# Kernel tuning notes

Hardware: AMD Instinct MI355X
Metric: run time of the kernel (lower is better)

Reference implementation:

```python
import jax, jax.numpy as jnp
import numpy as np

# Block-diagonal SplitMLP: fc1 group g sees [day | items[g]]; fc2 is purely per-group.
B, C, V, H, O, G = 128, 16, 32, 64, 4, 10000


def setup_inputs() -> dict:
    key = jax.random.key(0)
    ks = jax.random.split(key, 7)
    bound1 = 1.0 / np.sqrt(C + V * G)   # nn.Linear init bound for fc1 (full fan-in)
    bound2 = 1.0 / np.sqrt(H * G)       # fc2 fan-in
    return {
        "day": jax.random.normal(ks[0], (B, C), jnp.float32),
        "items": jax.random.normal(ks[1], (B, G, V), jnp.float32),
        "W1_day": jax.random.uniform(ks[2], (G, H, C), jnp.float32, -bound1, bound1),
        "W1_var": jax.random.uniform(ks[3], (G, H, V), jnp.float32, -bound1, bound1),
        "b1": jax.random.uniform(ks[4], (G, H), jnp.float32, -bound1, bound1),
        "W2": jax.random.uniform(ks[5], (G, O, H), jnp.float32, -bound2, bound2),
        "b2": jax.random.uniform(ks[6], (G, O), jnp.float32, -bound2, bound2),
    }


def reference(day, items, W1_day, W1_var, b1, W2, b2):
    # fc1: shared day columns + per-group var block, then ReLU
    h = (
        jnp.einsum("bc,ghc->bgh", day, W1_day)
        + jnp.einsum("bgv,ghv->bgh", items, W1_var)
        + b1
    )
    h = jax.nn.relu(h)
    # fc2: purely block-diagonal (num_const = 0)
    y = jnp.einsum("bgh,goh->bgo", h, W2) + b2  # (B, G, O)
    return y
```

## Files before the change

kernel.cpp:

```cpp
#include <hip/hip_runtime.h>
#include <hip/hip_bf16.h>


typedef __bf16 v8bf __attribute__((ext_vector_type(8)));
typedef __bf16 v4bf __attribute__((ext_vector_type(4)));
typedef float  v4f  __attribute__((ext_vector_type(4)));

#define B_   128
#define C_   16
#define V_   32
#define H_   64
#define O_   4
#define G_   10000
#define GPB  4
#define WS_  56
#define HS_  72
#define YS_  20

__device__ __forceinline__ v4bf cvt4(float4 f) {
  v4bf r;
  r[0] = (__bf16)f.x; r[1] = (__bf16)f.y; r[2] = (__bf16)f.z; r[3] = (__bf16)f.w;
  return r;
}
__device__ __forceinline__ v8bf cvt8(float4 lo, float4 hi) {
  v8bf r;
  r[0] = (__bf16)lo.x; r[1] = (__bf16)lo.y; r[2] = (__bf16)lo.z; r[3] = (__bf16)lo.w;
  r[4] = (__bf16)hi.x; r[5] = (__bf16)hi.y; r[6] = (__bf16)hi.z; r[7] = (__bf16)hi.w;
  return r;
}
__device__ __forceinline__ v8bf gload8(const float* __restrict__ p) {
  const float4* p4 = reinterpret_cast<const float4*>(p);
  return cvt8(p4[0], p4[1]);
}

__global__ __launch_bounds__(256, 4)
void splitmlp_kernel(const float* __restrict__ day,
                     const float* __restrict__ items,
                     const float* __restrict__ W1d,
                     const float* __restrict__ W1v,
                     const float* __restrict__ b1,
                     const float* __restrict__ W2,
                     const float* __restrict__ b2,
                     float* __restrict__ out) {
  __shared__ __bf16 W1s[H_ * WS_];
  __shared__ __bf16 Hb[4][32 * HS_];
  __shared__ float  Yb[B_ * YS_];

  const int t    = threadIdx.x;
  const int g0   = blockIdx.x * GPB;
  const int w    = t >> 6;
  const int lane = t & 63;
  const int c    = lane & 15;
  const int q    = lane >> 4;
  const int wbase = w * 32;

  v8bf zf;
#pragma unroll
  for (int i = 0; i < 8; ++i) zf[i] = (__bf16)0.0f;
  const v4f zero = {0.f, 0.f, 0.f, 0.f};

  float4 pd, pv0, pv1;
  {
    const float* W1dg = W1d + (size_t)g0 * (H_ * C_);
    const float* W1vg = W1v + (size_t)g0 * (H_ * V_);
    pd  = reinterpret_cast<const float4*>(W1dg)[t];
    pv0 = reinterpret_cast<const float4*>(W1vg)[t];
    pv1 = reinterpret_cast<const float4*>(W1vg)[t + 256];
  }

#pragma unroll 1
  for (int gi = 0; gi < GPB; ++gi) {
    const int g = g0 + gi;

    __syncthreads();
    {
      const int hd = t >> 2, kd = (t & 3) << 2;
      *reinterpret_cast<v4bf*>(&W1s[hd * WS_ + kd]) = cvt4(pd);
      const int hv0 = t >> 3, kv0 = C_ + ((t & 7) << 2);
      *reinterpret_cast<v4bf*>(&W1s[hv0 * WS_ + kv0]) = cvt4(pv0);
      const int i2 = t + 256;
      const int hv1 = i2 >> 3, kv1 = C_ + ((i2 & 7) << 2);
      *reinterpret_cast<v4bf*>(&W1s[hv1 * WS_ + kv1]) = cvt4(pv1);
    }
    if (gi < GPB - 1) {
      const float* W1dn = W1d + (size_t)(g + 1) * (H_ * C_);
      const float* W1vn = W1v + (size_t)(g + 1) * (H_ * V_);
      pd  = reinterpret_cast<const float4*>(W1dn)[t];
      pv0 = reinterpret_cast<const float4*>(W1vn)[t];
      pv1 = reinterpret_cast<const float4*>(W1vn)[t + 256];
    }
    __syncthreads();

    v8bf bfrag[2][2];
#pragma unroll
    for (int nb = 0; nb < 2; ++nb) {
      const int b = wbase + nb * 16 + c;
      const float* pit = items + (size_t)b * (G_ * V_) + (size_t)g * V_;
      const float* p0 = (q < 2) ? (day + b * C_ + q * 8) : (pit + (q - 2) * 8);
      bfrag[nb][0] = gload8(p0);
      bfrag[nb][1] = (q < 2) ? gload8(pit + 16 + q * 8) : zf;
    }

    v8bf wfrag[4][2];
#pragma unroll
    for (int m = 0; m < 4; ++m) {
      const int row = (m * 16 + c) * WS_;
      wfrag[m][0] = *reinterpret_cast<const v8bf*>(&W1s[row + q * 8]);
      wfrag[m][1] = (q < 2) ? *reinterpret_cast<const v8bf*>(&W1s[row + 32 + q * 8]) : zf;
    }

    v4f acc[4][2];
#pragma unroll
    for (int m = 0; m < 4; ++m)
#pragma unroll
      for (int nb = 0; nb < 2; ++nb) acc[m][nb] = zero;
#pragma unroll
    for (int m = 0; m < 4; ++m)
#pragma unroll
      for (int nb = 0; nb < 2; ++nb) {
        acc[m][nb] = __builtin_amdgcn_mfma_f32_16x16x32_bf16(wfrag[m][0], bfrag[nb][0], acc[m][nb], 0, 0, 0);
        acc[m][nb] = __builtin_amdgcn_mfma_f32_16x16x32_bf16(wfrag[m][1], bfrag[nb][1], acc[m][nb], 0, 0, 0);
      }

#pragma unroll
    for (int m = 0; m < 4; ++m) {
      const float4 bb = *reinterpret_cast<const float4*>(b1 + (size_t)g * H_ + m * 16 + q * 4);
#pragma unroll
      for (int nb = 0; nb < 2; ++nb) {
        v4bf hv;
        hv[0] = (__bf16)fmaxf(acc[m][nb][0] + bb.x, 0.f);
        hv[1] = (__bf16)fmaxf(acc[m][nb][1] + bb.y, 0.f);
        hv[2] = (__bf16)fmaxf(acc[m][nb][2] + bb.z, 0.f);
        hv[3] = (__bf16)fmaxf(acc[m][nb][3] + bb.w, 0.f);
        *reinterpret_cast<v4bf*>(&Hb[w][(nb * 16 + c) * HS_ + m * 16 + q * 4]) = hv;
      }
    }

    v4f y[2] = {zero, zero};
#pragma unroll
    for (int kt = 0; kt < 2; ++kt) {
      const float* pw2 = W2 + (size_t)g * (O_ * H_) + c * H_ + kt * 32 + q * 8;
      v8bf w2f = (c < O_) ? gload8(pw2) : zf;
#pragma unroll
      for (int nb = 0; nb < 2; ++nb) {
        v8bf hf = *reinterpret_cast<const v8bf*>(&Hb[w][(nb * 16 + c) * HS_ + kt * 32 + q * 8]);
        y[nb] = __builtin_amdgcn_mfma_f32_16x16x32_bf16(w2f, hf, y[nb], 0, 0, 0);
      }
    }

    if (q == 0) {
      const float4 b2v = *reinterpret_cast<const float4*>(b2 + (size_t)g * O_);
#pragma unroll
      for (int nb = 0; nb < 2; ++nb) {
        const int b = wbase + nb * 16 + c;
        float4 o;
        o.x = y[nb][0] + b2v.x;
        o.y = y[nb][1] + b2v.y;
        o.z = y[nb][2] + b2v.z;
        o.w = y[nb][3] + b2v.w;
        *reinterpret_cast<float4*>(&Yb[b * YS_ + gi * 4]) = o;
      }
    }
  }

  __syncthreads();
#pragma unroll
  for (int i = t; i < 512; i += 256) {
    const int b = i >> 2, c4 = i & 3;
    const float4 v = *reinterpret_cast<const float4*>(&Yb[b * YS_ + c4 * 4]);
    *reinterpret_cast<float4*>(out + (size_t)b * (G_ * O_) + (size_t)g0 * O_ + c4 * 4) = v;
  }
}

extern "C" void kernel_launch(void* const* d_in, const int* in_sizes, int n_in,
                              void* d_out, int out_size, void* d_ws, size_t ws_size,
                              hipStream_t stream) {
  const float* day   = (const float*)d_in[0];
  const float* items = (const float*)d_in[1];
  const float* W1d   = (const float*)d_in[2];
  const float* W1v   = (const float*)d_in[3];
  const float* b1    = (const float*)d_in[4];
  const float* W2    = (const float*)d_in[5];
  const float* b2    = (const float*)d_in[6];
  float* out = (float*)d_out;
  splitmlp_kernel<<<G_ / GPB, 256, 0, stream>>>(day, items, W1d, W1v, b1, W2, b2, out);
}
```

Before: 352.3 us.

## Prefetch items and biases across group iterations, hoist day fragments, relax barriers

Loads the day fragments once per block and prefetches the next group's items slice into registers while the current group's MFMAs run. b1 is staged through shared memory, W2 is loaded early in the iteration, and b2 is added in the final store loop. The full __syncthreads is replaced by an LDS-only waitcnt plus s_barrier, so outstanding global prefetches are not drained at each barrier. The aim is to hide global load latency, which dominates this memory-bound kernel, at the cost of higher register pressure.

```diff
diff --git a/kernel.cpp b/kernel.cpp
--- a/kernel.cpp
+++ b/kernel.cpp
@@ -43,6 +43,7 @@
                      const float* __restrict__ b2,
                      float* __restrict__ out) {
   __shared__ __bf16 W1s[H_ * WS_];
+  __shared__ float  B1s[H_];
   __shared__ __bf16 Hb[4][32 * HS_];
   __shared__ float  Yb[B_ * YS_];
 
@@ -59,20 +60,40 @@
   for (int i = 0; i < 8; ++i) zf[i] = (__bf16)0.0f;
   const v4f zero = {0.f, 0.f, 0.f, 0.f};
 
+  v8bf dayf[2];
+#pragma unroll
+  for (int nb = 0; nb < 2; ++nb) {
+    const int b = wbase + nb * 16 + c;
+    dayf[nb] = (q < 2) ? gload8(day + b * C_ + q * 8) : zf;
+  }
+
   float4 pd, pv0, pv1;
+  float  pb1;
   {
     const float* W1dg = W1d + (size_t)g0 * (H_ * C_);
     const float* W1vg = W1v + (size_t)g0 * (H_ * V_);
     pd  = reinterpret_cast<const float4*>(W1dg)[t];
     pv0 = reinterpret_cast<const float4*>(W1vg)[t];
     pv1 = reinterpret_cast<const float4*>(W1vg)[t + 256];
-  }
+    pb1 = b1[(size_t)g0 * H_ + (t & 63)];
+  }
+  const int ioff = ((q + 2) & 3) * 8;
+  const float* pit0 = items + (size_t)(wbase + c) * (G_ * V_) + (size_t)g0 * V_ + ioff;
+  const float* pit1 = pit0 + (size_t)16 * (G_ * V_);
+  float4 it[2][2];
+  it[0][0] = reinterpret_cast<const float4*>(pit0)[0];
+  it[0][1] = reinterpret_cast<const float4*>(pit0)[1];
+  it[1][0] = reinterpret_cast<const float4*>(pit1)[0];
+  it[1][1] = reinterpret_cast<const float4*>(pit1)[1];
 
 #pragma unroll 1
   for (int gi = 0; gi < GPB; ++gi) {
     const int g = g0 + gi;
 
-    __syncthreads();
+    asm volatile("s_waitcnt lgkmcnt(0)" ::: "memory");
+    __builtin_amdgcn_s_barrier();
+    asm volatile("" ::: "memory");
+
     {
       const int hd = t >> 2, kd = (t & 3) << 2;
       *reinterpret_cast<v4bf*>(&W1s[hd * WS_ + kd]) = cvt4(pd);
@@ -81,6 +102,16 @@
       const int i2 = t + 256;
       const int hv1 = i2 >> 3, kv1 = C_ + ((i2 & 7) << 2);
       *reinterpret_cast<v4bf*>(&W1s[hv1 * WS_ + kv1]) = cvt4(pv1);
+      if (t < H_) B1s[t] = pb1;
+    }
+
+    float4 w2r[2][2];
+    {
+      const float* pw2 = W2 + (size_t)g * (O_ * H_) + (c & 3) * H_ + q * 8;
+      w2r[0][0] = reinterpret_cast<const float4*>(pw2)[0];
+      w2r[0][1] = reinterpret_cast<const float4*>(pw2)[1];
+      w2r[1][0] = reinterpret_cast<const float4*>(pw2 + 32)[0];
+      w2r[1][1] = reinterpret_cast<const float4*>(pw2 + 32)[1];
     }
     if (gi < GPB - 1) {
       const float* W1dn = W1d + (size_t)(g + 1) * (H_ * C_);
@@ -88,43 +119,50 @@
       pd  = reinterpret_cast<const float4*>(W1dn)[t];
       pv0 = reinterpret_cast<const float4*>(W1vn)[t];
       pv1 = reinterpret_cast<const float4*>(W1vn)[t + 256];
-    }
-    __syncthreads();
-
-    v8bf bfrag[2][2];
+      pb1 = b1[(size_t)(g + 1) * H_ + (t & 63)];
+    }
+
+    asm volatile("s_waitcnt lgkmcnt(0)" ::: "memory");
+    __builtin_amdgcn_s_barrier();
+    asm volatile("" ::: "memory");
+
+    v8bf bl[2], bh[2];
 #pragma unroll
     for (int nb = 0; nb < 2; ++nb) {
-      const int b = wbase + nb * 16 + c;
-      const float* pit = items + (size_t)b * (G_ * V_) + (size_t)g * V_;
-      const float* p0 = (q < 2) ? (day + b * C_ + q * 8) : (pit + (q - 2) * 8);
-      bfrag[nb][0] = gload8(p0);
-      bfrag[nb][1] = (q < 2) ? gload8(pit + 16 + q * 8) : zf;
-    }
-
-    v8bf wfrag[4][2];
+      const v8bf ic = cvt8(it[nb][0], it[nb][1]);
+      bl[nb] = (q < 2) ? dayf[nb] : ic;
+      bh[nb] = (q < 2) ? ic : zf;
+    }
+
+    v4f acc[4][2];
+#pragma unroll
+    for (int m = 0; m < 4; ++m)
+#pragma unroll
+      for (int nb = 0; nb < 2; ++nb) acc[m][nb] = zero;
 #pragma unroll
     for (int m = 0; m < 4; ++m) {
       const int row = (m * 16 + c) * WS_;
-      wfrag[m][0] = *reinterpret_cast<const v8bf*>(&W1s[row + q * 8]);
-      wfrag[m][1] = (q < 2) ? *reinterpret_cast<const v8bf*>(&W1s[row + 32 + q * 8]) : zf;
-    }
-
-    v4f acc[4][2];
-#pragma unroll
-    for (int m = 0; m < 4; ++m)
-#pragma unroll
-      for (int nb = 0; nb < 2; ++nb) acc[m][nb] = zero;
-#pragma unroll
-    for (int m = 0; m < 4; ++m)
-#pragma unroll
-      for (int nb = 0; nb < 2; ++nb) {
-        acc[m][nb] = __builtin_amdgcn_mfma_f32_16x16x32_bf16(wfrag[m][0], bfrag[nb][0], acc[m][nb], 0, 0, 0);
-        acc[m][nb] = __builtin_amdgcn_mfma_f32_16x16x32_bf16(wfrag[m][1], bfrag[nb][1], acc[m][nb], 0, 0, 0);
-      }
+      const v8bf w0 = *reinterpret_cast<const v8bf*>(&W1s[row + q * 8]);
+      const v8bf w1 = (q < 2) ? *reinterpret_cast<const v8bf*>(&W1s[row + 32 + q * 8]) : zf;
+#pragma unroll
+      for (int nb = 0; nb < 2; ++nb) {
+        acc[m][nb] = __builtin_amdgcn_mfma_f32_16x16x32_bf16(w0, bl[nb], acc[m][nb], 0, 0, 0);
+        acc[m][nb] = __builtin_amdgcn_mfma_f32_16x16x32_bf16(w1, bh[nb], acc[m][nb], 0, 0, 0);
+      }
+    }
+
+    if (gi < GPB - 1) {
+      pit0 += V_;
+      pit1 += V_;
+      it[0][0] = reinterpret_cast<const float4*>(pit0)[0];
+      it[0][1] = reinterpret_cast<const float4*>(pit0)[1];
+      it[1][0] = reinterpret_cast<const float4*>(pit1)[0];
+      it[1][1] = reinterpret_cast<const float4*>(pit1)[1];
+    }
 
 #pragma unroll
     for (int m = 0; m < 4; ++m) {
-      const float4 bb = *reinterpret_cast<const float4*>(b1 + (size_t)g * H_ + m * 16 + q * 4);
+      const float4 bb = *reinterpret_cast<const float4*>(&B1s[m * 16 + q * 4]);
 #pragma unroll
       for (int nb = 0; nb < 2; ++nb) {
         v4bf hv;
@@ -139,25 +177,20 @@
     v4f y[2] = {zero, zero};
 #pragma unroll
     for (int kt = 0; kt < 2; ++kt) {
-      const float* pw2 = W2 + (size_t)g * (O_ * H_) + c * H_ + kt * 32 + q * 8;
-      v8bf w2f = (c < O_) ? gload8(pw2) : zf;
-#pragma unroll
-      for (int nb = 0; nb < 2; ++nb) {
-        v8bf hf = *reinterpret_cast<const v8bf*>(&Hb[w][(nb * 16 + c) * HS_ + kt * 32 + q * 8]);
+      const v8bf w2f = (c < O_) ? cvt8(w2r[kt][0], w2r[kt][1]) : zf;
+#pragma unroll
+      for (int nb = 0; nb < 2; ++nb) {
+        const v8bf hf = *reinterpret_cast<const v8bf*>(&Hb[w][(nb * 16 + c) * HS_ + kt * 32 + q * 8]);
         y[nb] = __builtin_amdgcn_mfma_f32_16x16x32_bf16(w2f, hf, y[nb], 0, 0, 0);
       }
     }
 
     if (q == 0) {
-      const float4 b2v = *reinterpret_cast<const float4*>(b2 + (size_t)g * O_);
 #pragma unroll
       for (int nb = 0; nb < 2; ++nb) {
         const int b = wbase + nb * 16 + c;
         float4 o;
-        o.x = y[nb][0] + b2v.x;
-        o.y = y[nb][1] + b2v.y;
-        o.z = y[nb][2] + b2v.z;
-        o.w = y[nb][3] + b2v.w;
+        o.x = y[nb][0]; o.y = y[nb][1]; o.z = y[nb][2]; o.w = y[nb][3];
         *reinterpret_cast<float4*>(&Yb[b * YS_ + gi * 4]) = o;
       }
     }
@@ -167,7 +200,9 @@
 #pragma unroll
   for (int i = t; i < 512; i += 256) {
     const int b = i >> 2, c4 = i & 3;
-    const float4 v = *reinterpret_cast<const float4*>(&Yb[b * YS_ + c4 * 4]);
+    const float4 bv = *reinterpret_cast<const float4*>(b2 + (size_t)(g0 + c4) * O_);
+    float4 v = *reinterpret_cast<const float4*>(&Yb[b * YS_ + c4 * 4]);
+    v.x += bv.x; v.y += bv.y; v.z += bv.z; v.w += bv.w;
     *reinterpret_cast<float4*>(out + (size_t)b * (G_ * O_) + (size_t)g0 * O_ + c4 * 4) = v;
   }
 }
```

Result: faster. 343.0 us (-2.7%).

## Assign one group per wave with register-resident weights and batch-chunk pipelining

Applied to the files above, without the earlier changes.

Restructures the kernel so each wave owns one group and keeps that group's W1, W2 and biases in registers, dropping the block-shared W1 staging in LDS and its per-group barriers. The wave walks the batch in 16-row chunks, prefetching the next chunk's items slice while computing the current one, and writes outputs straight to global memory instead of staging them through an LDS output buffer. The day matrix is staged once in LDS as bf16. In exchange the output stores become scattered 16-byte writes, and register pressure rises, which may lower occupancy.

```diff
diff --git a/kernel.cpp b/kernel.cpp
--- a/kernel.cpp
+++ b/kernel.cpp
@@ -13,9 +13,8 @@
 #define O_   4
 #define G_   10000
 #define GPB  4
-#define WS_  56
+#define DS_  24
 #define HS_  72
-#define YS_  20
 
 __device__ __forceinline__ v4bf cvt4(float4 f) {
   v4bf r;
@@ -28,10 +27,6 @@
   r[4] = (__bf16)hi.x; r[5] = (__bf16)hi.y; r[6] = (__bf16)hi.z; r[7] = (__bf16)hi.w;
   return r;
 }
-__device__ __forceinline__ v8bf gload8(const float* __restrict__ p) {
-  const float4* p4 = reinterpret_cast<const float4*>(p);
-  return cvt8(p4[0], p4[1]);
-}
 
 __global__ __launch_bounds__(256, 4)
 void splitmlp_kernel(const float* __restrict__ day,
@@ -42,134 +37,140 @@
                      const float* __restrict__ W2,
                      const float* __restrict__ b2,
                      float* __restrict__ out) {
-  __shared__ __bf16 W1s[H_ * WS_];
-  __shared__ __bf16 Hb[4][32 * HS_];
-  __shared__ float  Yb[B_ * YS_];
+  __shared__ __bf16 Dl[B_ * DS_];
+  __shared__ __bf16 Hb[4][16 * HS_];
 
   const int t    = threadIdx.x;
-  const int g0   = blockIdx.x * GPB;
   const int w    = t >> 6;
   const int lane = t & 63;
   const int c    = lane & 15;
   const int q    = lane >> 4;
-  const int wbase = w * 32;
+  const int g    = blockIdx.x * GPB + w;
 
   v8bf zf;
 #pragma unroll
   for (int i = 0; i < 8; ++i) zf[i] = (__bf16)0.0f;
   const v4f zero = {0.f, 0.f, 0.f, 0.f};
 
-  float4 pd, pv0, pv1;
+  float4 dd[2];
   {
-    const float* W1dg = W1d + (size_t)g0 * (H_ * C_);
-    const float* W1vg = W1v + (size_t)g0 * (H_ * V_);
-    pd  = reinterpret_cast<const float4*>(W1dg)[t];
-    pv0 = reinterpret_cast<const float4*>(W1vg)[t];
-    pv1 = reinterpret_cast<const float4*>(W1vg)[t + 256];
+    const float4* d4 = reinterpret_cast<const float4*>(day);
+    dd[0] = d4[t];
+    dd[1] = d4[t + 256];
   }
 
-#pragma unroll 1
-  for (int gi = 0; gi < GPB; ++gi) {
-    const int g = g0 + gi;
-
-    __syncthreads();
-    {
-      const int hd = t >> 2, kd = (t & 3) << 2;
-      *reinterpret_cast<v4bf*>(&W1s[hd * WS_ + kd]) = cvt4(pd);
-      const int hv0 = t >> 3, kv0 = C_ + ((t & 7) << 2);
-      *reinterpret_cast<v4bf*>(&W1s[hv0 * WS_ + kv0]) = cvt4(pv0);
-      const int i2 = t + 256;
-      const int hv1 = i2 >> 3, kv1 = C_ + ((i2 & 7) << 2);
-      *reinterpret_cast<v4bf*>(&W1s[hv1 * WS_ + kv1]) = cvt4(pv1);
-    }
-    if (gi < GPB - 1) {
-      const float* W1dn = W1d + (size_t)(g + 1) * (H_ * C_);
-      const float* W1vn = W1v + (size_t)(g + 1) * (H_ * V_);
-      pd  = reinterpret_cast<const float4*>(W1dn)[t];
-      pv0 = reinterpret_cast<const float4*>(W1vn)[t];
-      pv1 = reinterpret_cast<const float4*>(W1vn)[t + 256];
-    }
-    __syncthreads();
-
-    v8bf bfrag[2][2];
+  const float* W1dg = W1d + (size_t)g * (H_ * C_);
+  const float* W1vg = W1v + (size_t)g * (H_ * V_);
+  float4 s0[4][2], s1[4][2];
 #pragma unroll
-    for (int nb = 0; nb < 2; ++nb) {
-      const int b = wbase + nb * 16 + c;
-      const float* pit = items + (size_t)b * (G_ * V_) + (size_t)g * V_;
-      const float* p0 = (q < 2) ? (day + b * C_ + q * 8) : (pit + (q - 2) * 8);
-      bfrag[nb][0] = gload8(p0);
-      bfrag[nb][1] = (q < 2) ? gload8(pit + 16 + q * 8) : zf;
-    }
-
-    v8bf wfrag[4][2];
+  for (int m = 0; m < 4; ++m) {
+    const int h = m * 16 + c;
+    const float* p0 = (q < 2) ? (W1dg + h * C_ + q * 8) : (W1vg + h * V_ + (q - 2) * 8);
+    s0[m][0] = reinterpret_cast<const float4*>(p0)[0];
+    s0[m][1] = reinterpret_cast<const float4*>(p0)[1];
+  }
 #pragma unroll
-    for (int m = 0; m < 4; ++m) {
-      const int row = (m * 16 + c) * WS_;
-      wfrag[m][0] = *reinterpret_cast<const v8bf*>(&W1s[row + q * 8]);
-      wfrag[m][1] = (q < 2) ? *reinterpret_cast<const v8bf*>(&W1s[row + 32 + q * 8]) : zf;
-    }
-
-    v4f acc[4][2];
-#pragma unroll
-    for (int m = 0; m < 4; ++m)
-#pragma unroll
-      for (int nb = 0; nb < 2; ++nb) acc[m][nb] = zero;
-#pragma unroll
-    for (int m = 0; m < 4; ++m)
-#pragma unroll
-      for (int nb = 0; nb < 2; ++nb) {
-        acc[m][nb] = __builtin_amdgcn_mfma_f32_16x16x32_bf16(wfrag[m][0], bfrag[nb][0], acc[m][nb], 0, 0, 0);
-        acc[m][nb] = __builtin_amdgcn_mfma_f32_16x16x32_bf16(wfrag[m][1], bfrag[nb][1], acc[m][nb], 0, 0, 0);
-      }
-
-#pragma unroll
-    for (int m = 0; m < 4; ++m) {
-      const float4 bb = *reinterpret_cast<const float4*>(b1 + (size_t)g * H_ + m * 16 + q * 4);
-#pragma unroll
-      for (int nb = 0; nb < 2; ++nb) {
-        v4bf hv;
-        hv[0] = (__bf16)fmaxf(acc[m][nb][0] + bb.x, 0.f);
-        hv[1] = (__bf16)fmaxf(acc[m][nb][1] + bb.y, 0.f);
-        hv[2] = (__bf16)fmaxf(acc[m][nb][2] + bb.z, 0.f);
-        hv[3] = (__bf16)fmaxf(acc[m][nb][3] + bb.w, 0.f);
-        *reinterpret_cast<v4bf*>(&Hb[w][(nb * 16 + c) * HS_ + m * 16 + q * 4]) = hv;
-      }
-    }
-
-    v4f y[2] = {zero, zero};
-#pragma unroll
-    for (int kt = 0; kt < 2; ++kt) {
-      const float* pw2 = W2 + (size_t)g * (O_ * H_) + c * H_ + kt * 32 + q * 8;
-      v8bf w2f = (c < O_) ? gload8(pw2) : zf;
-#pragma unroll
-      for (int nb = 0; nb < 2; ++nb) {
-        v8bf hf = *reinterpret_cast<const v8bf*>(&Hb[w][(nb * 16 + c) * HS_ + kt * 32 + q * 8]);
-        y[nb] = __builtin_amdgcn_mfma_f32_16x16x32_bf16(w2f, hf, y[nb], 0, 0, 0);
-      }
-    }
-
-    if (q == 0) {
-      const float4 b2v = *reinterpret_cast<const float4*>(b2 + (size_t)g * O_);
-#pragma unroll
-      for (int nb = 0; nb < 2; ++nb) {
-        const int b = wbase + nb * 16 + c;
-        float4 o;
-        o.x = y[nb][0] + b2v.x;
-        o.y = y[nb][1] + b2v.y;
-        o.z = y[nb][2] + b2v.z;
-        o.w = y[nb][3] + b2v.w;
-        *reinterpret_cast<float4*>(&Yb[b * YS_ + gi * 4]) = o;
-      }
+  for (int m = 0; m < 4; ++m) {
+    if (q < 2) {
+      const float* p1 = W1vg + (m * 16 + c) * V_ + 16 + q * 8;
+      s1[m][0] = reinterpret_cast<const float4*>(p1)[0];
+      s1[m][1] = reinterpret_cast<const float4*>(p1)[1];
     }
   }
+  float4 w2s[2][2];
+  {
+    const float* pw2 = W2 + (size_t)g * (O_ * H_) + (c & 3) * H_ + q * 8;
+    w2s[0][0] = reinterpret_cast<const float4*>(pw2)[0];
+    w2s[0][1] = reinterpret_cast<const float4*>(pw2)[1];
+    w2s[1][0] = reinterpret_cast<const float4*>(pw2 + 32)[0];
+    w2s[1][1] = reinterpret_cast<const float4*>(pw2 + 32)[1];
+  }
+  float4 bb[4];
+#pragma unroll
+  for (int m = 0; m < 4; ++m)
+    bb[m] = *reinterpret_cast<const float4*>(b1 + (size_t)g * H_ + m * 16 + q * 4);
+  const float4 b2v = *reinterpret_cast<const float4*>(b2 + (size_t)g * O_);
 
-  __syncthreads();
+  const int ioff = ((q + 2) & 3) * 8;
+  const float* itbase = items + (size_t)c * (G_ * V_) + (size_t)g * V_ + ioff;
+  float4 itA[2], itB[2];
+  itA[0] = reinterpret_cast<const float4*>(itbase)[0];
+  itA[1] = reinterpret_cast<const float4*>(itbase)[1];
+
+  {
 #pragma unroll
-  for (int i = t; i < 512; i += 256) {
-    const int b = i >> 2, c4 = i & 3;
-    const float4 v = *reinterpret_cast<const float4*>(&Yb[b * YS_ + c4 * 4]);
-    *reinterpret_cast<float4*>(out + (size_t)b * (G_ * O_) + (size_t)g0 * O_ + c4 * 4) = v;
+    for (int i = 0; i < 2; ++i) {
+      const int idx = t + i * 256;
+      const int b = idx >> 2, col = (idx & 3) << 2;
+      *reinterpret_cast<v4bf*>(&Dl[b * DS_ + col]) = cvt4(dd[i]);
+    }
   }
+  asm volatile("s_waitcnt lgkmcnt(0)" ::: "memory");
+  __builtin_amdgcn_s_barrier();
+  asm volatile("" ::: "memory");
+
+  v8bf wf0[4], wf1[4], w2f[2];
+#pragma unroll
+  for (int m = 0; m < 4; ++m) wf0[m] = cvt8(s0[m][0], s0[m][1]);
+#pragma unroll
+  for (int m = 0; m < 4; ++m) wf1[m] = (q < 2) ? cvt8(s1[m][0], s1[m][1]) : zf;
+  w2f[0] = (c < O_) ? cvt8(w2s[0][0], w2s[0][1]) : zf;
+  w2f[1] = (c < O_) ? cvt8(w2s[1][0], w2s[1][1]) : zf;
+
+#define CHUNK(CH, CUR, NXT, PREF)                                              \
+  {                                                                            \
+    if (PREF) {                                                                \
+      const float* p = itbase + (size_t)(((CH) + 1) * 16) * (G_ * V_);         \
+      NXT[0] = reinterpret_cast<const float4*>(p)[0];                          \
+      NXT[1] = reinterpret_cast<const float4*>(p)[1];                          \
+    }                                                                          \
+    const v8bf dayv =                                                          \
+        *reinterpret_cast<const v8bf*>(&Dl[((CH) * 16 + c) * DS_ + (q & 1) * 8]); \
+    const v8bf ic  = cvt8(CUR[0], CUR[1]);                                     \
+    const v8bf blv = (q < 2) ? dayv : ic;                                      \
+    const v8bf bhv = (q < 2) ? ic : zf;                                        \
+    v4f acc[4];                                                                \
+    _Pragma("unroll")                                                          \
+    for (int m = 0; m < 4; ++m) acc[m] = zero;                                 \
+    _Pragma("unroll")                                                          \
+    for (int m = 0; m < 4; ++m) {                                              \
+      acc[m] = __builtin_amdgcn_mfma_f32_16x16x32_bf16(wf0[m], blv, acc[m], 0, 0, 0); \
+      acc[m] = __builtin_amdgcn_mfma_f32_16x16x32_bf16(wf1[m], bhv, acc[m], 0, 0, 0); \
+    }                                                                          \
+    _Pragma("unroll")                                                          \
+    for (int m = 0; m < 4; ++m) {                                              \
+      v4bf hv;                                                                 \
+      hv[0] = (__bf16)fmaxf(acc[m][0] + bb[m].x, 0.f);                         \
+      hv[1] = (__bf16)fmaxf(acc[m][1] + bb[m].y, 0.f);                         \
+      hv[2] = (__bf16)fmaxf(acc[m][2] + bb[m].z, 0.f);                         \
+      hv[3] = (__bf16)fmaxf(acc[m][3] + bb[m].w, 0.f);                         \
+      *reinterpret_cast<v4bf*>(&Hb[w][c * HS_ + m * 16 + q * 4]) = hv;         \
+    }                                                                          \
+    v4f y = zero;                                                              \
+    _Pragma("unroll")                                                          \
+    for (int kt = 0; kt < 2; ++kt) {                                           \
+      const v8bf hf =                                                          \
+          *reinterpret_cast<const v8bf*>(&Hb[w][c * HS_ + kt * 32 + q * 8]);   \
+      y = __builtin_amdgcn_mfma_f32_16x16x32_bf16(w2f[kt], hf, y, 0, 0, 0);    \
+    }                                                                          \
+    if (q == 0) {                                                              \
+      float4 o;                                                                \
+      o.x = y[0] + b2v.x; o.y = y[1] + b2v.y;                                  \
+      o.z = y[2] + b2v.z; o.w = y[3] + b2v.w;                                  \
+      *reinterpret_cast<float4*>(out + (size_t)((CH) * 16 + c) * (G_ * O_) +   \
+                                 (size_t)g * O_) = o;                          \
+    }                                                                          \
+  }
+
+  CHUNK(0, itA, itB, 1)
+  CHUNK(1, itB, itA, 1)
+  CHUNK(2, itA, itB, 1)
+  CHUNK(3, itB, itA, 1)
+  CHUNK(4, itA, itB, 1)
+  CHUNK(5, itB, itA, 1)
+  CHUNK(6, itA, itB, 1)
+  CHUNK(7, itB, itA, 0)
+#undef CHUNK
 }
 
 extern "C" void kernel_launch(void* const* d_in, const int* in_sizes, int n_in,
```

Result: faster. 338.9 us (-3.8%).

## Load W1 fragments directly to registers and software-pipeline all per-group loads

Applied to the files above, without the earlier changes.

Drops the shared-memory staging of W1 and both block-wide barriers per group. Each lane now loads its MFMA weight fragments straight from global memory and prefetches the next group's W1, W2, items and bias values during the current group's compute. Groups per block go from 4 to 8, day fragments are hoisted out of the loop, and outputs are written directly to global instead of through a shared buffer. The cost is much higher register pressure (launch bounds lowered to 2 blocks per CU), fewer blocks, and scattered 16-byte output stores.

```diff
diff --git a/kernel.cpp b/kernel.cpp
--- a/kernel.cpp
+++ b/kernel.cpp
@@ -12,16 +12,9 @@
 #define H_   64
 #define O_   4
 #define G_   10000
-#define GPB  4
-#define WS_  56
+#define NG   8
 #define HS_  72
-#define YS_  20
 
-__device__ __forceinline__ v4bf cvt4(float4 f) {
-  v4bf r;
-  r[0] = (__bf16)f.x; r[1] = (__bf16)f.y; r[2] = (__bf16)f.z; r[3] = (__bf16)f.w;
-  return r;
-}
 __device__ __forceinline__ v8bf cvt8(float4 lo, float4 hi) {
   v8bf r;
   r[0] = (__bf16)lo.x; r[1] = (__bf16)lo.y; r[2] = (__bf16)lo.z; r[3] = (__bf16)lo.w;
@@ -33,7 +26,7 @@
   return cvt8(p4[0], p4[1]);
 }
 
-__global__ __launch_bounds__(256, 4)
+__global__ __launch_bounds__(256, 2)
 void splitmlp_kernel(const float* __restrict__ day,
                      const float* __restrict__ items,
                      const float* __restrict__ W1d,
@@ -42,73 +35,100 @@
                      const float* __restrict__ W2,
                      const float* __restrict__ b2,
                      float* __restrict__ out) {
-  __shared__ __bf16 W1s[H_ * WS_];
   __shared__ __bf16 Hb[4][32 * HS_];
-  __shared__ float  Yb[B_ * YS_];
 
   const int t    = threadIdx.x;
-  const int g0   = blockIdx.x * GPB;
   const int w    = t >> 6;
   const int lane = t & 63;
   const int c    = lane & 15;
   const int q    = lane >> 4;
-  const int wbase = w * 32;
+  const int g0   = blockIdx.x * NG;
+  const int rbase = w * 32;
 
   v8bf zf;
 #pragma unroll
   for (int i = 0; i < 8; ++i) zf[i] = (__bf16)0.0f;
   const v4f zero = {0.f, 0.f, 0.f, 0.f};
 
-  float4 pd, pv0, pv1;
-  {
-    const float* W1dg = W1d + (size_t)g0 * (H_ * C_);
-    const float* W1vg = W1v + (size_t)g0 * (H_ * V_);
-    pd  = reinterpret_cast<const float4*>(W1dg)[t];
-    pv0 = reinterpret_cast<const float4*>(W1vg)[t];
-    pv1 = reinterpret_cast<const float4*>(W1vg)[t + 256];
+  v8bf dayf[2];
+#pragma unroll
+  for (int nb = 0; nb < 2; ++nb) {
+    const int b = rbase + nb * 16 + c;
+    dayf[nb] = (q < 2) ? gload8(day + b * C_ + q * 8) : zf;
   }
 
+  const float* p0 = (q < 2) ? (W1d + (size_t)g0 * (H_ * C_) + c * C_ + q * 8)
+                            : (W1v + (size_t)g0 * (H_ * V_) + c * V_ + (q - 2) * 8);
+  const int ms0 = (q < 2) ? (16 * C_) : (16 * V_);
+  const int st0 = (q < 2) ? (H_ * C_) : (H_ * V_);
+  const float* p1 = W1v + (size_t)g0 * (H_ * V_) + c * V_ + 16 + q * 8;
+  const float* pw2 = W2 + (size_t)g0 * (O_ * H_) + (c & 3) * H_ + q * 8;
+  const int ioff = ((q + 2) & 3) * 8;
+  const float* pit = items + (size_t)(rbase + c) * (G_ * V_) + (size_t)g0 * V_ + ioff;
+  const float* pb1 = b1 + (size_t)g0 * H_;
+  const float* pb2 = b2 + (size_t)g0 * O_;
+
+  float4 s0[4][2], s1[4][2], w2s[2][2], it[2][2];
+
+#define ISSUE()                                                        \
+  {                                                                    \
+    _Pragma("unroll")                                                  \
+    for (int m = 0; m < 4; ++m) {                                      \
+      const float* p = p0 + m * ms0;                                   \
+      s0[m][0] = reinterpret_cast<const float4*>(p)[0];                \
+      s0[m][1] = reinterpret_cast<const float4*>(p)[1];                \
+    }                                                                  \
+    if (q < 2) {                                                       \
+      _Pragma("unroll")                                                \
+      for (int m = 0; m < 4; ++m) {                                    \
+        const float* p = p1 + m * (16 * V_);                           \
+        s1[m][0] = reinterpret_cast<const float4*>(p)[0];              \
+        s1[m][1] = reinterpret_cast<const float4*>(p)[1];              \
+      }                                                                \
+    }                                                                  \
+    w2s[0][0] = reinterpret_cast<const float4*>(pw2)[0];               \
+    w2s[0][1] = reinterpret_cast<const float4*>(pw2)[1];               \
+    w2s[1][0] = reinterpret_cast<const float4*>(pw2 + 32)[0];          \
+    w2s[1][1] = reinterpret_cast<const float4*>(pw2 + 32)[1];          \
+    it[0][0] = reinterpret_cast<const float4*>(pit)[0];                \
+    it[0][1] = reinterpret_cast<const float4*>(pit)[1];                \
+    {                                                                  \
+      const float* pitB = pit + (size_t)16 * (G_ * V_);                \
+      it[1][0] = reinterpret_cast<const float4*>(pitB)[0];             \
+      it[1][1] = reinterpret_cast<const float4*>(pitB)[1];             \
+    }                                                                  \
+    p0 += st0; p1 += H_ * V_; pw2 += O_ * H_; pit += V_;               \
+  }
+
+  ISSUE();
+
 #pragma unroll 1
-  for (int gi = 0; gi < GPB; ++gi) {
-    const int g = g0 + gi;
+  for (int gi = 0; gi < NG; ++gi) {
+    v8bf wf0[4], wf1[4], w2f[2], icf[2];
+#pragma unroll
+    for (int m = 0; m < 4; ++m) wf0[m] = cvt8(s0[m][0], s0[m][1]);
+#pragma unroll
+    for (int m = 0; m < 4; ++m) wf1[m] = (q < 2) ? cvt8(s1[m][0], s1[m][1]) : zf;
+    w2f[0] = (c < O_) ? cvt8(w2s[0][0], w2s[0][1]) : zf;
+    w2f[1] = (c < O_) ? cvt8(w2s[1][0], w2s[1][1]) : zf;
+#pragma unroll
+    for (int nb = 0; nb < 2; ++nb) icf[nb] = cvt8(it[nb][0], it[nb][1]);
 
-    __syncthreads();
-    {
-      const int hd = t >> 2, kd = (t & 3) << 2;
-      *reinterpret_cast<v4bf*>(&W1s[hd * WS_ + kd]) = cvt4(pd);
-      const int hv0 = t >> 3, kv0 = C_ + ((t & 7) << 2);
-      *reinterpret_cast<v4bf*>(&W1s[hv0 * WS_ + kv0]) = cvt4(pv0);
-      const int i2 = t + 256;
-      const int hv1 = i2 >> 3, kv1 = C_ + ((i2 & 7) << 2);
-      *reinterpret_cast<v4bf*>(&W1s[hv1 * WS_ + kv1]) = cvt4(pv1);
-    }
-    if (gi < GPB - 1) {
-      const float* W1dn = W1d + (size_t)(g + 1) * (H_ * C_);
-      const float* W1vn = W1v + (size_t)(g + 1) * (H_ * V_);
-      pd  = reinterpret_cast<const float4*>(W1dn)[t];
-      pv0 = reinterpret_cast<const float4*>(W1vn)[t];
-      pv1 = reinterpret_cast<const float4*>(W1vn)[t + 256];
-    }
-    __syncthreads();
+    float4 bbv[4];
+#pragma unroll
+    for (int m = 0; m < 4; ++m)
+      bbv[m] = *reinterpret_cast<const float4*>(pb1 + m * 16 + q * 4);
+    const float4 b2v = *reinterpret_cast<const float4*>(pb2);
+    pb1 += H_; pb2 += O_;
 
-    v8bf bfrag[2][2];
+    if (gi < NG - 1) ISSUE();
+
+    v8bf blv[2], bhv[2];
 #pragma unroll
     for (int nb = 0; nb < 2; ++nb) {
-      const int b = wbase + nb * 16 + c;
-      const float* pit = items + (size_t)b * (G_ * V_) + (size_t)g * V_;
-      const float* p0 = (q < 2) ? (day + b * C_ + q * 8) : (pit + (q - 2) * 8);
-      bfrag[nb][0] = gload8(p0);
-      bfrag[nb][1] = (q < 2) ? gload8(pit + 16 + q * 8) : zf;
+      blv[nb] = (q < 2) ? dayf[nb] : icf[nb];
+      bhv[nb] = (q < 2) ? icf[nb] : zf;
     }
-
-    v8bf wfrag[4][2];
-#pragma unroll
-    for (int m = 0; m < 4; ++m) {
-      const int row = (m * 16 + c) * WS_;
-      wfrag[m][0] = *reinterpret_cast<const v8bf*>(&W1s[row + q * 8]);
-      wfrag[m][1] = (q < 2) ? *reinterpret_cast<const v8bf*>(&W1s[row + 32 + q * 8]) : zf;
-    }
-
     v4f acc[4][2];
 #pragma unroll
     for (int m = 0; m < 4; ++m)
@@ -118,58 +138,45 @@
     for (int m = 0; m < 4; ++m)
 #pragma unroll
       for (int nb = 0; nb < 2; ++nb) {
-        acc[m][nb] = __builtin_amdgcn_mfma_f32_16x16x32_bf16(wfrag[m][0], bfrag[nb][0], acc[m][nb], 0, 0, 0);
-        acc[m][nb] = __builtin_amdgcn_mfma_f32_16x16x32_bf16(wfrag[m][1], bfrag[nb][1], acc[m][nb], 0, 0, 0);
+        acc[m][nb] = __builtin_amdgcn_mfma_f32_16x16x32_bf16(wf0[m], blv[nb], acc[m][nb], 0, 0, 0);
+        acc[m][nb] = __builtin_amdgcn_mfma_f32_16x16x32_bf16(wf1[m], bhv[nb], acc[m][nb], 0, 0, 0);
       }
 
 #pragma unroll
-    for (int m = 0; m < 4; ++m) {
-      const float4 bb = *reinterpret_cast<const float4*>(b1 + (size_t)g * H_ + m * 16 + q * 4);
+    for (int m = 0; m < 4; ++m)
 #pragma unroll
       for (int nb = 0; nb < 2; ++nb) {
         v4bf hv;
-        hv[0] = (__bf16)fmaxf(acc[m][nb][0] + bb.x, 0.f);
-        hv[1] = (__bf16)fmaxf(acc[m][nb][1] + bb.y, 0.f);
-        hv[2] = (__bf16)fmaxf(acc[m][nb][2] + bb.z, 0.f);
-        hv[3] = (__bf16)fmaxf(acc[m][nb][3] + bb.w, 0.f);
+        hv[0] = (__bf16)fmaxf(acc[m][nb][0] + bbv[m].x, 0.f);
+        hv[1] = (__bf16)fmaxf(acc[m][nb][1] + bbv[m].y, 0.f);
+        hv[2] = (__bf16)fmaxf(acc[m][nb][2] + bbv[m].z, 0.f);
+        hv[3] = (__bf16)fmaxf(acc[m][nb][3] + bbv[m].w, 0.f);
         *reinterpret_cast<v4bf*>(&Hb[w][(nb * 16 + c) * HS_ + m * 16 + q * 4]) = hv;
       }
-    }
 
     v4f y[2] = {zero, zero};
 #pragma unroll
-    for (int kt = 0; kt < 2; ++kt) {
-      const float* pw2 = W2 + (size_t)g * (O_ * H_) + c * H_ + kt * 32 + q * 8;
-      v8bf w2f = (c < O_) ? gload8(pw2) : zf;
+    for (int kt = 0; kt < 2; ++kt)
 #pragma unroll
       for (int nb = 0; nb < 2; ++nb) {
-        v8bf hf = *reinterpret_cast<const v8bf*>(&Hb[w][(nb * 16 + c) * HS_ + kt * 32 + q * 8]);
-        y[nb] = __builtin_amdgcn_mfma_f32_16x16x32_bf16(w2f, hf, y[nb], 0, 0, 0);
+        const v8bf hf = *reinterpret_cast<const v8bf*>(&Hb[w][(nb * 16 + c) * HS_ + kt * 32 + q * 8]);
+        y[nb] = __builtin_amdgcn_mfma_f32_16x16x32_bf16(w2f[kt], hf, y[nb], 0, 0, 0);
       }
-    }
 
     if (q == 0) {
-      const float4 b2v = *reinterpret_cast<const float4*>(b2 + (size_t)g * O_);
 #pragma unroll
       for (int nb = 0; nb < 2; ++nb) {
-        const int b = wbase + nb * 16 + c;
         float4 o;
         o.x = y[nb][0] + b2v.x;
         o.y = y[nb][1] + b2v.y;
         o.z = y[nb][2] + b2v.z;
         o.w = y[nb][3] + b2v.w;
-        *reinterpret_cast<float4*>(&Yb[b * YS_ + gi * 4]) = o;
+        *reinterpret_cast<float4*>(out + (size_t)(rbase + nb * 16 + c) * (G_ * O_) +
+                                   (size_t)(g0 + gi) * O_) = o;
       }
     }
   }
-
-  __syncthreads();
-#pragma unroll
-  for (int i = t; i < 512; i += 256) {
-    const int b = i >> 2, c4 = i & 3;
-    const float4 v = *reinterpret_cast<const float4*>(&Yb[b * YS_ + c4 * 4]);
-    *reinterpret_cast<float4*>(out + (size_t)b * (G_ * O_) + (size_t)g0 * O_ + c4 * 4) = v;
-  }
+#undef ISSUE
 }
 
 extern "C" void kernel_launch(void* const* d_in, const int* in_sizes, int n_in,
@@ -183,5 +190,5 @@
   const float* W2    = (const float*)d_in[5];
   const float* b2    = (const float*)d_in[6];
   float* out = (float*)d_out;
-  splitmlp_kernel<<<G_ / GPB, 256, 0, stream>>>(day, items, W1d, W1v, b1, W2, b2, out);
+  splitmlp_kernel<<<G_ / NG, 256, 0, stream>>>(day, items, W1d, W1v, b1, W2, b2, out);
 }
```

Result: slower. 368.7 us (+4.6%).
